# Optimization experiments

Hardware: AMD Instinct MI355X
Metric: run time of the kernel (lower is better)

Reference implementation:

```python
import jax, jax.numpy as jnp
import numpy as np

B, S, C = 4, 4096, 1024
H, D, K = 16, 64, 256  # nhead, head_dim, dim_k


def setup_inputs() -> dict:
    key = jax.random.key(0)
    ks = jax.random.split(key, 7)
    x = jax.random.normal(ks[0], (B, S, C), dtype=jnp.float32)
    # per-head QKV projection weights (torch Linear weight layout [out,in])
    Wq = jax.random.normal(ks[1], (H, D, C), dtype=jnp.float32) * (C ** -0.5)
    Wk = jax.random.normal(ks[2], (H, D, C), dtype=jnp.float32) * (C ** -0.5)
    Wv = jax.random.normal(ks[3], (H, D, C), dtype=jnp.float32) * (C ** -0.5)
    # Linformer E/F sequence projections, per head: [K, S]
    We = jax.random.normal(ks[4], (H, K, S), dtype=jnp.float32) * (S ** -0.5)
    Wf = jax.random.normal(ks[5], (H, K, S), dtype=jnp.float32) * (S ** -0.5)
    # output projection (with bias, as w_o is nn.Linear default bias=True)
    Wo = jax.random.normal(ks[6], (C, H * D), dtype=jnp.float32) * ((H * D) ** -0.5)
    bo = jnp.zeros((C,), dtype=jnp.float32)
    return {"x": x, "Wq": Wq, "Wk": Wk, "Wv": Wv, "We": We, "Wf": Wf, "Wo": Wo, "bo": bo}


def reference(x, Wq, Wk, Wv, We, Wf, Wo, bo):
    # per-head projections: [B,H,S,D]
    Q = jnp.einsum('bsc,hdc->bhsd', x, Wq)
    Kh = jnp.einsum('bsc,hdc->bhsd', x, Wk)
    Vh = jnp.einsum('bsc,hdc->bhsd', x, Wv)
    # E-projection of K over the sequence axis: K^T [B,H,D,S] -> [B,H,D,K]
    Kp = jnp.einsum('bhsd,hks->bhdk', Kh, We)
    # scores: Q @ E(K^T) / sqrt(head_dim), softmax over low-rank axis k
    scale = 1.0 / jnp.sqrt(jnp.asarray(D, dtype=x.dtype))
    P = jax.nn.softmax(jnp.einsum('bhsd,bhdk->bhsk', Q, Kp) * scale, axis=-1)
    # F-projection of V over the sequence axis, then transpose back: [B,H,K,D]
    Vp = jnp.einsum('bhsd,hks->bhkd', Vh, Wf)
    out = jnp.einsum('bhsk,bhkd->bhsd', P, Vp)          # [B,H,S,D]
    out = out.transpose(0, 2, 1, 3).reshape(B, S, H * D)  # concat heads
    return jnp.einsum('bse,ce->bsc', out, Wo) + bo       # w_o (dropout=0)
```

## Files before the change

kernel.cpp:

```cpp
#include <hip/hip_runtime.h>
#include <stdint.h>


typedef unsigned short u16;
typedef __bf16 bf16t;
typedef bf16t bf16x8 __attribute__((ext_vector_type(8)));
typedef float f32x4 __attribute__((ext_vector_type(4)));
typedef u16 u16x8 __attribute__((ext_vector_type(8)));

#define MFMA16(a, b, c) __builtin_amdgcn_mfma_f32_16x16x32_bf16((a), (b), (c), 0, 0, 0)

__device__ __forceinline__ u16 f2bf(float f) {
  return __builtin_bit_cast(u16, (bf16t)f);
}

__device__ __forceinline__ bf16x8 ldf(const u16* p) { return *(const bf16x8*)p; }

__device__ __forceinline__ void gload16(const void* g, void* l) {
  __builtin_amdgcn_global_load_lds(
      (__attribute__((address_space(1))) void*)g,
      (__attribute__((address_space(3))) void*)l, 16, 0, 0);
}

__device__ __forceinline__ int xcd_swz(int orig, int nwg) {
  return (orig & 7) * (nwg >> 3) + (orig >> 3);
}

#define FENCE asm volatile("" ::: "memory")
#define BAR                                  \
  do {                                       \
    FENCE;                                   \
    __builtin_amdgcn_s_barrier();            \
    FENCE;                                   \
  } while (0)

__device__ __forceinline__ void gemm256_pipe(const u16* __restrict__ A,
                                             const u16* __restrict__ B,
                                             int m0, int n0, int sA1, int sB1,
                                             int s0, int kt0, f32x4 acc[8][4],
                                             char* smc) {
  const int tid = threadIdx.x;
  const int w = tid >> 6, l = tid & 63, g = l >> 4, r = l & 15;
  const int wr = w >> 2, wc = w & 3;
  const int lrow = l >> 2;
  const int ksw = (((l & 3) ^ ((l >> 3) & 3)) << 4);
  const int gx = ((g ^ ((r >> 1) & 3)) << 4);

  auto stage = [&](const u16* Base, int r0, int s1, int T, int ch, int ldsoff) {
#pragma unroll
    for (int i = 0; i < 2; ++i) {
      const int row = r0 + (w * 2 + i) * 16 + lrow;
      const size_t eoff = (size_t)(row >> 6) * s1 + (size_t)(row & 63) * s0;
      gload16((const char*)Base + eoff * 2 + ((kt0 + T) * 64 + ch * 32) * 2 + ksw,
              smc + ldsoff + (w * 2 + i) * 1024);
    }
  };

#define RD_B(dst, Bt)                                                     \
  _Pragma("unroll") for (int n = 0; n < 4; ++n)                           \
      dst[n] = *(const bf16x8*)((Bt) + (wc * 64 + n * 16 + r) * 64 + gx);
#define RD_A(dst, At, MH)                                                 \
  _Pragma("unroll") for (int m = 0; m < 4; ++m)                           \
      dst[m] = *(const bf16x8*)((At) + (wr * 128 + (MH)*64 + m * 16 + r) * 64 + gx);
#define QUAD(MH)                                                          \
  __builtin_amdgcn_s_setprio(1);                                          \
  _Pragma("unroll") for (int m = 0; m < 4; ++m)                           \
      _Pragma("unroll") for (int n = 0; n < 4; ++n)                       \
          acc[(MH)*4 + m][n] = MFMA16(af[m], bfv[n], acc[(MH)*4 + m][n]); \
  __builtin_amdgcn_s_setprio(0);

  stage(B, n0, sB1, 0, 0, 0 + 32768);
  stage(A, m0, sA1, 0, 0, 0 + 0);
  stage(B, n0, sB1, 0, 1, 0 + 49152);
  stage(A, m0, sA1, 0, 1, 0 + 16384);
  stage(B, n0, sB1, 1, 0, 65536 + 32768);
  stage(A, m0, sA1, 1, 0, 65536 + 0);
  stage(B, n0, sB1, 1, 1, 65536 + 49152);
  asm volatile("s_waitcnt vmcnt(10)" ::: "memory");
  BAR;

  for (int t = 0; t < 16; ++t) {
    const int buf = (t & 1) << 16, nb = buf ^ 65536;
    const int T1 = t < 15 ? t + 1 : 15;
    const int T2 = t < 14 ? t + 2 : 15;
    bf16x8 af[4], bfv[4];
    const char* At0 = smc + buf;
    const char* At1 = smc + buf + 16384;
    const char* Bt0 = smc + buf + 32768;
    const char* Bt1 = smc + buf + 49152;

    RD_B(bfv, Bt0)
    RD_A(af, At0, 0)
    stage(A, m0, sA1, T1, 1, nb + 16384);
    BAR;
    QUAD(0)
    BAR;
    RD_A(af, At0, 1)
    stage(B, n0, sB1, T2, 0, buf + 32768);
    asm volatile("s_waitcnt vmcnt(10)" ::: "memory");
    BAR;
    QUAD(1)
    BAR;
    RD_B(bfv, Bt1)
    RD_A(af, At1, 0)
    stage(A, m0, sA1, T2, 0, buf + 0);
    BAR;
    QUAD(0)
    BAR;
    RD_A(af, At1, 1)
    stage(B, n0, sB1, T2, 1, buf + 49152);
    asm volatile("s_waitcnt vmcnt(10)" ::: "memory");
    BAR;
    QUAD(1)
    BAR;
  }
#undef RD_B
#undef RD_A
#undef QUAD
}

__global__ __launch_bounds__(256) void cvt_all(
    const float* __restrict__ x, const float* __restrict__ Wq,
    const float* __restrict__ Wk, const float* __restrict__ Wv,
    const float* __restrict__ Wo, u16* __restrict__ xb, u16* __restrict__ wqkv,
    u16* __restrict__ wob) {
  const int i = blockIdx.x * 256 + threadIdx.x;
  const float* s;
  u16* d;
  int off;
  if (i < 2097152) {
    s = x; d = xb; off = i;
  } else {
    const int j = i - 2097152, sel = j >> 17;
    off = j & 131071;
    if (sel == 0)      { s = Wq; d = wqkv; }
    else if (sel == 1) { s = Wk; d = wqkv + 1048576; }
    else if (sel == 2) { s = Wv; d = wqkv + 2097152; }
    else               { s = Wo; d = wob; }
  }
  const size_t e = (size_t)off * 8;
  const float4 a = *(const float4*)(s + e);
  const float4 b = *(const float4*)(s + e + 4);
  u16x8 o;
  o[0] = f2bf(a.x); o[1] = f2bf(a.y); o[2] = f2bf(a.z); o[3] = f2bf(a.w);
  o[4] = f2bf(b.x); o[5] = f2bf(b.y); o[6] = f2bf(b.z); o[7] = f2bf(b.w);
  *(u16x8*)(d + e) = o;
}

__global__ __launch_bounds__(512, 2) void gemm_qkv(const u16* __restrict__ xb,
                                                   const u16* __restrict__ wqkv,
                                                   u16* __restrict__ Qd,
                                                   u16* __restrict__ KTd,
                                                   u16* __restrict__ VTd) {
  __shared__ u16 sm[65536];
  const int tid = threadIdx.x, w = tid >> 6, l = tid & 63, g = l >> 4, r = l & 15;
  const int wr = w >> 2, wc = w & 3;
  f32x4 acc[8][4] = {};
  if (blockIdx.x < 512) {
    const int wg = xcd_swz(blockIdx.x, 512);
    const int m0 = (wg & 7) * 256, n0 = (wg >> 3) * 256;
    gemm256_pipe(wqkv + 1048576, xb, m0, n0, 65536, 65536, 1024, 0, acc, (char*)sm);
#pragma unroll
    for (int m = 0; m < 8; ++m)
#pragma unroll
      for (int n = 0; n < 4; ++n)
#pragma unroll
        for (int j = 0; j < 4; ++j) {
          const int mm = m0 + wr * 128 + m * 16 + g * 4 + j;
          const int nn = n0 + wc * 64 + n * 16 + r;
          const int which = mm >> 10, hd = mm & 1023, h = hd >> 6, d = hd & 63;
          const int b = nn >> 12, s = nn & 4095;
          u16* dst = which ? VTd : KTd;
          dst[(((size_t)(b * 16 + h)) * 64 + d) * 4096 + s] = f2bf(acc[m][n][j]);
        }
  } else {
    const int wg = xcd_swz(blockIdx.x - 512, 256);
    const int m0 = (wg >> 2) * 256, n0 = (wg & 3) * 256;
    gemm256_pipe(xb, wqkv, m0, n0, 65536, 65536, 1024, 0, acc, (char*)sm);
#pragma unroll
    for (int m = 0; m < 8; ++m)
#pragma unroll
      for (int n = 0; n < 4; ++n)
#pragma unroll
        for (int j = 0; j < 4; ++j) {
          const int mm = m0 + wr * 128 + m * 16 + g * 4 + j;
          const int nn = n0 + wc * 64 + n * 16 + r;
          const int b = mm >> 12, s = mm & 4095, h = nn >> 6, d = nn & 63;
          Qd[(((size_t)(b * 16 + h)) * 4096 + s) * 64 + d] =
              f2bf(acc[m][n][j] * 0.125f);
        }
  }
}

__global__ __launch_bounds__(512, 2) void gemm_out(const u16* __restrict__ A,
                                                   const u16* __restrict__ BT,
                                                   const float* __restrict__ bo,
                                                   float* __restrict__ out) {
  __shared__ u16 sm[65536];
  const int wg = xcd_swz(blockIdx.x, 256);
  const int m0 = (wg >> 2) * 256, n0 = (wg & 3) * 256;
  const int tid = threadIdx.x, w = tid >> 6, l = tid & 63, g = l >> 4, r = l & 15;
  const int wr = w >> 2, wc = w & 3;
  f32x4 acc[8][4] = {};
  gemm256_pipe(A, BT, m0, n0, 65536, 65536, 1024, 0, acc, (char*)sm);
#pragma unroll
  for (int m = 0; m < 8; ++m)
#pragma unroll
    for (int n = 0; n < 4; ++n)
#pragma unroll
      for (int j = 0; j < 4; ++j) {
        const int mm = m0 + wr * 128 + m * 16 + g * 4 + j;
        const int nn = n0 + wc * 64 + n * 16 + r;
        out[(size_t)mm * 1024 + nn] = acc[m][n][j] + bo[nn];
      }
}

__global__ __launch_bounds__(512, 2) void gemm_small(const float* __restrict__ WeF,
                                                     const float* __restrict__ WfF,
                                                     const u16* __restrict__ KT,
                                                     const u16* __restrict__ VT,
                                                     float* __restrict__ part) {
  __shared__ u16 sm[65536];
  char* smc = (char*)sm;
  const int bx = blockIdx.x;
  const int h = bx & 15, mode = (bx >> 4) & 1, chunk = bx >> 5;
  const float* Wp = (mode == 0 ? WeF : WfF) + (size_t)h * 1048576;
  const u16* Gp = (mode == 0 ? KT : VT) + (size_t)h * 262144;
  const int tid = threadIdx.x, w = tid >> 6, l = tid & 63, g = l >> 4, r = l & 15;
  const int wr = w >> 2, wc = w & 3;
  const int xc = (tid & 7) ^ ((tid >> 3) & 7);
  const int aR = tid >> 1;
  const int aS0 = (tid & 1) * 4;

  auto stageX = [&](int kt, int buf) {
#pragma unroll
    for (int i = 0; i < 4; ++i) {
      const int row = i * 64 + (tid >> 3);
      const int b = row >> 6, d = row & 63;
      gload16(Gp + (size_t)b * 4194304 + (size_t)d * 4096 + kt * 64 + xc * 8,
              smc + buf * 65536 + i * 8192 + tid * 16);
    }
  };
  float4 aw[8];
  auto loadY = [&](int kt) {
#pragma unroll
    for (int q = 0; q < 4; ++q) {
      const float* p = Wp + (size_t)aR * 4096 + kt * 64 + (aS0 + q) * 8;
      aw[q * 2 + 0] = *(const float4*)(p);
      aw[q * 2 + 1] = *(const float4*)(p + 4);
    }
  };
  auto writeY = [&](int buf) {
#pragma unroll
    for (int q = 0; q < 4; ++q) {
      const float* f0 = (const float*)&aw[q * 2];
      const float* f1 = (const float*)&aw[q * 2 + 1];
      u16x8 o;
#pragma unroll
      for (int e = 0; e < 4; ++e) {
        o[e] = f2bf(f0[e]);
        o[e + 4] = f2bf(f1[e]);
      }
      *(u16x8*)(smc + buf * 65536 + 32768 + aR * 128 +
                (((aS0 + q) ^ (aR & 7)) << 4)) = o;
    }
  };

  f32x4 acc[8][4] = {};
  auto compute = [&](int buf) {
    const char* X = smc + buf * 65536;
    const char* Y = X + 32768;
    const char* Ar = (mode == 0) ? Y : X;
    const char* Br = (mode == 0) ? X : Y;
#pragma unroll
    for (int kk = 0; kk < 2; ++kk) {
      bf16x8 af[8], bfv[4];
#pragma unroll
      for (int n = 0; n < 4; ++n) {
        const int row = wc * 64 + n * 16 + r;
        bfv[n] = *(const bf16x8*)(Br + row * 128 + (((kk * 4 + g) ^ (r & 7)) << 4));
      }
#pragma unroll
      for (int m = 0; m < 8; ++m) {
        const int row = wr * 128 + m * 16 + r;
        af[m] = *(const bf16x8*)(Ar + row * 128 + (((kk * 4 + g) ^ (r & 7)) << 4));
      }
      __builtin_amdgcn_s_setprio(1);
#pragma unroll
      for (int m = 0; m < 8; ++m)
#pragma unroll
        for (int n = 0; n < 4; ++n)
          acc[m][n] = MFMA16(af[m], bfv[n], acc[m][n]);
      __builtin_amdgcn_s_setprio(0);
    }
  };

  const int kt0 = chunk * 8;
  stageX(kt0, 0);
  loadY(kt0);
  asm volatile("s_waitcnt vmcnt(0)" ::: "memory");
  writeY(0);
  __syncthreads();
  for (int t = 0; t < 8; ++t) {
    const int buf = t & 1;
    if (t < 7) {
      stageX(kt0 + t + 1, buf ^ 1);
      loadY(kt0 + t + 1);
    }
    compute(buf);
    if (t < 7) {
      asm volatile("s_waitcnt vmcnt(0)" ::: "memory");
      writeY(buf ^ 1);
    }
    __syncthreads();
  }

  float* Cp = part + ((size_t)((mode * 8 + chunk) * 16 + h)) * 65536;
#pragma unroll
  for (int m = 0; m < 8; ++m)
#pragma unroll
    for (int n = 0; n < 4; ++n)
#pragma unroll
      for (int j = 0; j < 4; ++j)
        Cp[(size_t)(wr * 128 + m * 16 + g * 4 + j) * 256 + wc * 64 + n * 16 + r] =
            acc[m][n][j];
}

__global__ __launch_bounds__(256) void reduce_small(const float* __restrict__ part,
                                                    u16* __restrict__ Kp,
                                                    u16* __restrict__ VpT) {
  const int i = blockIdx.x * 256 + threadIdx.x;
  const int mode = i >> 18;
  const int rem = i & 262143;
  const int h = rem >> 14;
  const int e = (rem & 16383) * 4;
  const int m = e >> 8, n = e & 255;
  const float* pb = part + ((size_t)mode * 128 + h) * 65536 + e;
  float4 acc = *(const float4*)(pb);
#pragma unroll
  for (int c = 1; c < 8; ++c) {
    const float4 s = *(const float4*)(pb + (size_t)c * 1048576);
    acc.x += s.x; acc.y += s.y; acc.z += s.z; acc.w += s.w;
  }
  ushort4 o;
  o.x = f2bf(acc.x); o.y = f2bf(acc.y); o.z = f2bf(acc.z); o.w = f2bf(acc.w);
  if (mode == 0) {
    const int b = n >> 6, d = n & 63;
    *(ushort4*)(Kp + ((size_t)(b * 16 + h)) * 16384 + m * 64 + d) = o;
  } else {
    const int b = m >> 6, d = m & 63;
    *(ushort4*)(VpT + ((size_t)(b * 16 + h)) * 16384 + d * 256 + n) = o;
  }
}

__global__ __launch_bounds__(256, 1) void attn_fused(const u16* __restrict__ Q,
                                                     const u16* __restrict__ Kp,
                                                     const u16* __restrict__ VpT,
                                                     u16* __restrict__ att) {
  __shared__ u16 P[4][16 * 264];
  const int gid = blockIdx.x;
  const int bh = gid >> 3;
  const int st = gid & 7;
  const int hh = bh & 15, b = bh >> 4;
  const int tid = threadIdx.x, w = tid >> 6, l = tid & 63, g = l >> 4, r = l & 15;
  const u16* Kpb = Kp + (size_t)bh * 256 * 64;
  const u16* Vb = VpT + (size_t)bh * 64 * 256;

  bf16x8 kf[32];
  bf16x8 vf[32];
#pragma unroll
  for (int fn = 0; fn < 16; ++fn) {
    kf[fn * 2 + 0] = ldf(Kpb + (fn * 16 + r) * 64 + g * 8);
    kf[fn * 2 + 1] = ldf(Kpb + (fn * 16 + r) * 64 + 32 + g * 8);
  }
#pragma unroll
  for (int fn2 = 0; fn2 < 4; ++fn2)
#pragma unroll
    for (int kk = 0; kk < 8; ++kk)
      vf[fn2 * 8 + kk] = ldf(Vb + (fn2 * 16 + r) * 256 + kk * 32 + g * 8);

  u16* Pw = P[w];
  for (int t = 0; t < 8; ++t) {
    const int s0 = st * 512 + t * 64 + w * 16;
    const u16* Qb = Q + ((size_t)bh * 4096 + s0) * 64;
    const bf16x8 qf0 = ldf(Qb + r * 64 + g * 8);
    const bf16x8 qf1 = ldf(Qb + r * 64 + 32 + g * 8);
    f32x4 sc[16];
#pragma unroll
    for (int fn = 0; fn < 16; ++fn) {
      sc[fn] = MFMA16(qf0, kf[fn * 2 + 0], (f32x4){});
      sc[fn] = MFMA16(qf1, kf[fn * 2 + 1], sc[fn]);
    }
    float rinv[4];
#pragma unroll
    for (int j = 0; j < 4; ++j) {
      float sum = 0.f;
#pragma unroll
      for (int fn = 0; fn < 16; ++fn) {
        const float e = __expf(sc[fn][j]);
        sc[fn][j] = e;
        sum += e;
      }
      sum += __shfl_xor(sum, 1);
      sum += __shfl_xor(sum, 2);
      sum += __shfl_xor(sum, 4);
      sum += __shfl_xor(sum, 8);
      rinv[j] = 1.0f / sum;
    }
#pragma unroll
    for (int fn = 0; fn < 16; ++fn)
#pragma unroll
      for (int j = 0; j < 4; ++j)
        Pw[(g * 4 + j) * 264 + fn * 16 + r] = f2bf(sc[fn][j]);

    f32x4 o[4] = {};
#pragma unroll
    for (int kk = 0; kk < 8; ++kk) {
      const bf16x8 pa = ldf(Pw + r * 264 + kk * 32 + g * 8);
#pragma unroll
      for (int fn2 = 0; fn2 < 4; ++fn2)
        o[fn2] = MFMA16(pa, vf[fn2 * 8 + kk], o[fn2]);
    }
#pragma unroll
    for (int fn2 = 0; fn2 < 4; ++fn2)
#pragma unroll
      for (int j = 0; j < 4; ++j) {
        const int s = s0 + g * 4 + j;
        const int d = fn2 * 16 + r;
        att[((size_t)b * 4096 + s) * 1024 + hh * 64 + d] = f2bf(o[fn2][j] * rinv[j]);
      }
  }
}

extern "C" void kernel_launch(void* const* d_in, const int* in_sizes, int n_in,
                              void* d_out, int out_size, void* d_ws, size_t ws_size,
                              hipStream_t stream) {
  (void)in_sizes; (void)n_in; (void)out_size; (void)ws_size;
  const float* x  = (const float*)d_in[0];
  const float* Wq = (const float*)d_in[1];
  const float* Wk = (const float*)d_in[2];
  const float* Wv = (const float*)d_in[3];
  const float* We = (const float*)d_in[4];
  const float* Wf = (const float*)d_in[5];
  const float* Wo = (const float*)d_in[6];
  const float* bo = (const float*)d_in[7];
  char* ws = (char*)d_ws;
  u16* xb    = (u16*)(ws + 0);
  float* prt = (float*)(ws + 0);
  u16* wqkv  = (u16*)(ws + 33554432);
  u16* att   = (u16*)(ws + 73400320);
  u16* wob   = (u16*)(ws + 106954752);
  u16* Qd    = (u16*)(ws + 109051904);
  u16* KTd   = (u16*)(ws + 142606336);
  u16* VTd   = (u16*)(ws + 176160768);
  u16* Kpd   = (u16*)(ws + 209715200);
  u16* VpTd  = (u16*)(ws + 211812352);

  cvt_all<<<10240, 256, 0, stream>>>(x, Wq, Wk, Wv, Wo, xb, wqkv, wob);
  gemm_qkv<<<768, 512, 0, stream>>>(xb, wqkv, Qd, KTd, VTd);
  gemm_small<<<256, 512, 0, stream>>>(We, Wf, KTd, VTd, prt);
  reduce_small<<<2048, 256, 0, stream>>>(prt, Kpd, VpTd);
  attn_fused<<<512, 256, 0, stream>>>(Qd, Kpd, VpTd, att);
  gemm_out<<<256, 512, 0, stream>>>(att, wob, bo, (float*)d_out);
}
```

Measured before the change: 307.7 us.

## Load GEMM B operand directly into registers, stage only A in LDS

Replaces the shared 256x256 GEMM mainloop, which staged both A and B tiles into LDS, with a variant that stages only A in a swizzled double-buffered LDS layout. B fragments are loaded straight from global memory into registers, double-buffered across K steps. The change halves LDS usage to 64KB per block and removes B LDS traffic, aiming to raise occupancy and cut LDS bandwidth and barrier pressure. In exchange it increases register pressure and relies on uncoalesced per-lane global loads of B with less latency hiding. It also drops the general stride parameters, since all callers use the same contiguous layout.

```diff
diff --git a/kernel.cpp b/kernel.cpp
--- a/kernel.cpp
+++ b/kernel.cpp
@@ -34,89 +34,86 @@
     FENCE;                                   \
   } while (0)
 
-__device__ __forceinline__ void gemm256_pipe(const u16* __restrict__ A,
+__device__ __forceinline__ void gemm256_breg(const u16* __restrict__ A,
                                              const u16* __restrict__ B,
-                                             int m0, int n0, int sA1, int sB1,
-                                             int s0, int kt0, f32x4 acc[8][4],
+                                             int m0, int n0, f32x4 acc[8][4],
                                              char* smc) {
   const int tid = threadIdx.x;
   const int w = tid >> 6, l = tid & 63, g = l >> 4, r = l & 15;
   const int wr = w >> 2, wc = w & 3;
-  const int lrow = l >> 2;
-  const int ksw = (((l & 3) ^ ((l >> 3) & 3)) << 4);
-  const int gx = ((g ^ ((r >> 1) & 3)) << 4);
-
-  auto stage = [&](const u16* Base, int r0, int s1, int T, int ch, int ldsoff) {
-#pragma unroll
-    for (int i = 0; i < 2; ++i) {
-      const int row = r0 + (w * 2 + i) * 16 + lrow;
-      const size_t eoff = (size_t)(row >> 6) * s1 + (size_t)(row & 63) * s0;
-      gload16((const char*)Base + eoff * 2 + ((kt0 + T) * 64 + ch * 32) * 2 + ksw,
-              smc + ldsoff + (w * 2 + i) * 1024);
+  const int arow = tid >> 3;
+  const int ac = tid & 7;
+
+  auto stageA = [&](int T, int buf) {
+#pragma unroll
+    for (int i = 0; i < 4; ++i) {
+      const int row = i * 64 + arow;
+      const int sc = ac ^ (row & 7);
+      gload16((const char*)A + (size_t)(m0 + row) * 2048 + T * 128 + sc * 16,
+              smc + buf * 32768 + i * 8192 + tid * 16);
     }
   };
 
-#define RD_B(dst, Bt)                                                     \
-  _Pragma("unroll") for (int n = 0; n < 4; ++n)                           \
-      dst[n] = *(const bf16x8*)((Bt) + (wc * 64 + n * 16 + r) * 64 + gx);
-#define RD_A(dst, At, MH)                                                 \
-  _Pragma("unroll") for (int m = 0; m < 4; ++m)                           \
-      dst[m] = *(const bf16x8*)((At) + (wr * 128 + (MH)*64 + m * 16 + r) * 64 + gx);
-#define QUAD(MH)                                                          \
-  __builtin_amdgcn_s_setprio(1);                                          \
-  _Pragma("unroll") for (int m = 0; m < 4; ++m)                           \
-      _Pragma("unroll") for (int n = 0; n < 4; ++n)                       \
-          acc[(MH)*4 + m][n] = MFMA16(af[m], bfv[n], acc[(MH)*4 + m][n]); \
-  __builtin_amdgcn_s_setprio(0);
-
-  stage(B, n0, sB1, 0, 0, 0 + 32768);
-  stage(A, m0, sA1, 0, 0, 0 + 0);
-  stage(B, n0, sB1, 0, 1, 0 + 49152);
-  stage(A, m0, sA1, 0, 1, 0 + 16384);
-  stage(B, n0, sB1, 1, 0, 65536 + 32768);
-  stage(A, m0, sA1, 1, 0, 65536 + 0);
-  stage(B, n0, sB1, 1, 1, 65536 + 49152);
-  asm volatile("s_waitcnt vmcnt(10)" ::: "memory");
+#define LOADB(T, bv)                                                          \
+  _Pragma("unroll") for (int kk = 0; kk < 2; ++kk)                            \
+      _Pragma("unroll") for (int n = 0; n < 4; ++n)                           \
+          bv[kk * 4 + n] = *(const bf16x8*)((const char*)B +                  \
+              (size_t)(n0 + wc * 64 + n * 16 + r) * 2048 + (T)*128 +          \
+              kk * 64 + g * 16);
+
+#define COMPUTE(buf, bv)                                                      \
+  {                                                                           \
+    const char* At = smc + (buf)*32768;                                       \
+    _Pragma("unroll") for (int kk = 0; kk < 2; ++kk) {                        \
+      bf16x8 af[8];                                                           \
+      _Pragma("unroll") for (int m = 0; m < 8; ++m) {                         \
+        const int R = wr * 128 + m * 16 + r;                                  \
+        af[m] = *(const bf16x8*)(At + R * 128 + (((kk * 4 + g) ^ (r & 7)) << 4)); \
+      }                                                                       \
+      __builtin_amdgcn_s_setprio(1);                                          \
+      _Pragma("unroll") for (int m = 0; m < 8; ++m)                           \
+          _Pragma("unroll") for (int n = 0; n < 4; ++n)                       \
+              acc[m][n] = MFMA16(af[m], bv[kk * 4 + n], acc[m][n]);           \
+      __builtin_amdgcn_s_setprio(0);                                          \
+    }                                                                         \
+  }
+
+  bf16x8 b0[8], b1[8];
+  stageA(0, 0);
+  stageA(1, 1);
+  LOADB(0, b0)
+  asm volatile("s_waitcnt vmcnt(12)" ::: "memory");
   BAR;
 
-  for (int t = 0; t < 16; ++t) {
-    const int buf = (t & 1) << 16, nb = buf ^ 65536;
-    const int T1 = t < 15 ? t + 1 : 15;
-    const int T2 = t < 14 ? t + 2 : 15;
-    bf16x8 af[4], bfv[4];
-    const char* At0 = smc + buf;
-    const char* At1 = smc + buf + 16384;
-    const char* Bt0 = smc + buf + 32768;
-    const char* Bt1 = smc + buf + 49152;
-
-    RD_B(bfv, Bt0)
-    RD_A(af, At0, 0)
-    stage(A, m0, sA1, T1, 1, nb + 16384);
+#pragma unroll 1
+  for (int t = 0; t < 16; t += 2) {
+    {
+      const int Tb = t + 1;
+      LOADB(Tb, b1)
+    }
+    COMPUTE(0, b0)
     BAR;
-    QUAD(0)
+    {
+      const int Ta = t + 2 < 16 ? t + 2 : 15;
+      stageA(Ta, 0);
+    }
+    asm volatile("s_waitcnt vmcnt(12)" ::: "memory");
     BAR;
-    RD_A(af, At0, 1)
-    stage(B, n0, sB1, T2, 0, buf + 32768);
-    asm volatile("s_waitcnt vmcnt(10)" ::: "memory");
+    {
+      const int Tb = t + 2 < 16 ? t + 2 : 15;
+      LOADB(Tb, b0)
+    }
+    COMPUTE(1, b1)
     BAR;
-    QUAD(1)
+    {
+      const int Ta = t + 3 < 16 ? t + 3 : 15;
+      stageA(Ta, 1);
+    }
+    asm volatile("s_waitcnt vmcnt(12)" ::: "memory");
     BAR;
-    RD_B(bfv, Bt1)
-    RD_A(af, At1, 0)
-    stage(A, m0, sA1, T2, 0, buf + 0);
-    BAR;
-    QUAD(0)
-    BAR;
-    RD_A(af, At1, 1)
-    stage(B, n0, sB1, T2, 1, buf + 49152);
-    asm volatile("s_waitcnt vmcnt(10)" ::: "memory");
-    BAR;
-    QUAD(1)
-    BAR;
-  }
-#undef RD_B
-#undef RD_A
-#undef QUAD
+  }
+#undef LOADB
+#undef COMPUTE
 }
 
 __global__ __launch_bounds__(256) void cvt_all(
@@ -152,14 +149,14 @@
                                                    u16* __restrict__ Qd,
                                                    u16* __restrict__ KTd,
                                                    u16* __restrict__ VTd) {
-  __shared__ u16 sm[65536];
+  __shared__ u16 sm[32768];
   const int tid = threadIdx.x, w = tid >> 6, l = tid & 63, g = l >> 4, r = l & 15;
   const int wr = w >> 2, wc = w & 3;
   f32x4 acc[8][4] = {};
   if (blockIdx.x < 512) {
     const int wg = xcd_swz(blockIdx.x, 512);
     const int m0 = (wg & 7) * 256, n0 = (wg >> 3) * 256;
-    gemm256_pipe(wqkv + 1048576, xb, m0, n0, 65536, 65536, 1024, 0, acc, (char*)sm);
+    gemm256_breg(wqkv + 1048576, xb, m0, n0, acc, (char*)sm);
 #pragma unroll
     for (int m = 0; m < 8; ++m)
 #pragma unroll
@@ -176,7 +173,7 @@
   } else {
     const int wg = xcd_swz(blockIdx.x - 512, 256);
     const int m0 = (wg >> 2) * 256, n0 = (wg & 3) * 256;
-    gemm256_pipe(xb, wqkv, m0, n0, 65536, 65536, 1024, 0, acc, (char*)sm);
+    gemm256_breg(xb, wqkv, m0, n0, acc, (char*)sm);
 #pragma unroll
     for (int m = 0; m < 8; ++m)
 #pragma unroll
@@ -196,13 +193,13 @@
                                                    const u16* __restrict__ BT,
                                                    const float* __restrict__ bo,
                                                    float* __restrict__ out) {
-  __shared__ u16 sm[65536];
+  __shared__ u16 sm[32768];
   const int wg = xcd_swz(blockIdx.x, 256);
   const int m0 = (wg >> 2) * 256, n0 = (wg & 3) * 256;
   const int tid = threadIdx.x, w = tid >> 6, l = tid & 63, g = l >> 4, r = l & 15;
   const int wr = w >> 2, wc = w & 3;
   f32x4 acc[8][4] = {};
-  gemm256_pipe(A, BT, m0, n0, 65536, 65536, 1024, 0, acc, (char*)sm);
+  gemm256_breg(A, BT, m0, n0, acc, (char*)sm);
 #pragma unroll
   for (int m = 0; m < 8; ++m)
 #pragma unroll
```

New measurement: 392.2 us. 27.4% more time.
